# Optimization experiments

Measured on AMD Instinct MI355X. Metric: run time of the kernel, lower is better.

The kernel has to match this reference:

```python
import jax, jax.numpy as jnp
import numpy as np
import math

SEQ, BSZ, D, H, W = 2048, 2, 1024, 16, 8
HD = D // H          # head_dim = 64
P = SEQ // W         # phrase_num = 256 (seq divisible by window -> no pad needed)


def setup_inputs() -> dict:
    key = jax.random.key(0)
    ks = jax.random.split(key, 8)
    s = 1.0 / math.sqrt(D)
    def w(k):
        return jax.random.normal(k, (D, D), jnp.float32) * s
    zb = jnp.zeros((D,), jnp.float32)
    return {
        'query': jax.random.normal(ks[0], (SEQ, BSZ, D), jnp.float32),
        'Wq_base': w(ks[1]), 'bq_base': zb,
        'Wk_base': w(ks[2]), 'bk_base': zb,
        'Wq_gauss': w(ks[3]), 'bq_gauss': zb,
        'Wk_gauss': w(ks[4]), 'bk_gauss': zb,
        'Wv': w(ks[5]), 'bv': zb,
        'Wo': w(ks[6]), 'bo': zb,
    }


def reference(query, Wq_base, bq_base, Wk_base, bk_base,
              Wq_gauss, bq_gauss, Wk_gauss, bk_gauss, Wv, bv, Wo, bo):
    seq, bsz, d = query.shape
    scaling = HD ** -0.5

    def to_heads(x):  # (len, bsz, D) -> (bsz, H, len, HD)
        return x.reshape(x.shape[0], bsz, H, HD).transpose(1, 2, 0, 3)

    # ---- base multi-head attention branch ----
    q_b = to_heads(query @ Wq_base.T + bq_base) * scaling
    k_b = to_heads(query @ Wk_base.T + bk_base)
    v = to_heads(query @ Wv.T + bv)
    base_scores = jnp.einsum('bhid,bhjd->bhij', q_b, k_b)   # (B,H,S,S)
    attn_base = jax.nn.softmax(base_scores, axis=-1)

    # ---- phrase encoding: fixed windows + max pooling ----
    phrase = query.reshape(P, W, bsz, d).max(axis=1)        # (P, bsz, D)

    # ---- gaussian branch: query attends over phrase reps ----
    q_g = to_heads(query @ Wq_gauss.T + bq_gauss) * scaling
    k_g = (phrase @ Wk_gauss.T + bk_gauss).reshape(P, bsz, H, HD).transpose(1, 2, 0, 3)
    wts = jax.nn.softmax(jnp.einsum('bhid,bhpd->bhip', q_g, k_g), axis=-1)  # (B,H,S,P)

    # fixed Gaussians per phrase: mu at window center, sigma = window/4
    pos = jnp.arange(seq, dtype=jnp.float32)                     # key positions
    mu = jnp.arange(P, dtype=jnp.float32) * W + (W - 1) / 2.0    # (P,)
    sigma = W / 4.0
    gauss = jnp.exp(-(pos[None, :] - mu[:, None]) ** 2 / (2.0 * sigma * sigma)) \
            / (math.sqrt(2.0 * math.pi) * sigma)                 # (P, S)
    attn_gauss = jnp.einsum('bhip,pj->bhij', wts, gauss)         # (B,H,S,S)

    # combine the two attention distributions
    attn = 0.5 * (attn_base + attn_gauss)

    out = jnp.einsum('bhij,bhjd->bhid', attn, v)                 # (B,H,S,HD)
    out = out.transpose(2, 0, 1, 3).reshape(seq, bsz, d)         # (S,B,D)
    return out @ Wo.T + bo
```

## Files before the change

kernel.cpp:

```cpp
#include <hip/hip_runtime.h>
#include <hip/hip_bf16.h>

#define SEQ 2048
#define BSZ 2
#define DIM 1024
#define NH 16
#define HD 64
#define WIN 8
#define PN 256

typedef __hip_bfloat16 bf16;
typedef __attribute__((ext_vector_type(8))) short short8;
typedef __attribute__((ext_vector_type(4))) float f32x4;

__device__ __forceinline__ float b2f(bf16 x) { return __bfloat162float(x); }
__device__ __forceinline__ bf16 f2b(float x) { return __float2bfloat16(x); }
__device__ __forceinline__ short fbits(float x) { bf16 h = __float2bfloat16(x); return *(short*)&h; }

__device__ __forceinline__ void gl_lds16(const bf16* g, bf16* l) {
    __builtin_amdgcn_global_load_lds((const __attribute__((address_space(1))) void*)g,
                                     (__attribute__((address_space(3))) void*)l, 16, 0, 0);
}

__global__ void convert_kernel(const float* __restrict__ q,
                               const float* __restrict__ w0, const float* __restrict__ w1,
                               const float* __restrict__ w2, const float* __restrict__ w3,
                               const float* __restrict__ w4, const float* __restrict__ w5,
                               bf16* __restrict__ qbf, bf16* __restrict__ wbf) {
    int i = blockIdx.x * 256 + threadIdx.x;
    const int QV = (SEQ * BSZ * DIM) / 8;
    const int WV = (DIM * DIM) / 8;
    const float* src;
    bf16* dst;
    size_t off;
    if (i < QV) { src = q; dst = qbf; off = (size_t)i * 8; }
    else {
        int j = i - QV;
        int mat = j / WV, k = j - mat * WV;
        src = (mat == 0) ? w0 : (mat == 1) ? w1 : (mat == 2) ? w2
            : (mat == 3) ? w3 : (mat == 4) ? w4 : w5;
        dst = wbf + (size_t)mat * DIM * DIM;
        off = (size_t)k * 8;
    }
    f32x4 a = *(const f32x4*)(src + off);
    f32x4 b4 = *(const f32x4*)(src + off + 4);
    short8 o;
#pragma unroll
    for (int e = 0; e < 4; ++e) { o[e] = fbits(a[e]); o[e + 4] = fbits(b4[e]); }
    *(short8*)(dst + off) = o;
}

__global__ void bias_pack_kernel(const float* __restrict__ b0, const float* __restrict__ b1,
                                 const float* __restrict__ b2, const float* __restrict__ b3,
                                 const float* __restrict__ b4, const float* __restrict__ b5,
                                 float* __restrict__ bp) {
    int i = blockIdx.x * 256 + threadIdx.x;
    int mat = i >> 10, k = i & 1023;
    const float* s = (mat == 0) ? b0 : (mat == 1) ? b1 : (mat == 2) ? b2
                   : (mat == 3) ? b3 : (mat == 4) ? b4 : b5;
    bp[i] = s[k];
}

__global__ void phrase_max_kernel(const float* __restrict__ q, bf16* __restrict__ phrase) {
    int idx = blockIdx.x * 256 + threadIdx.x;
    int d  = idx % DIM;
    int pb = idx / DIM;
    int b  = pb % BSZ;
    int p  = pb / BSZ;
    float m = -1e30f;
#pragma unroll
    for (int w = 0; w < WIN; ++w)
        m = fmaxf(m, q[((size_t)(p * WIN + w) * BSZ + b) * DIM + d]);
    phrase[idx] = f2b(m);
}

__global__ void gauss_v_kernel(const bf16* __restrict__ vT, bf16* __restrict__ gvT) {
    int row = blockIdx.x;
    int p   = threadIdx.x;
    float mu = p * (float)WIN + (WIN - 1) * 0.5f;
    float acc = 0.f;
    int j0 = p * WIN - 12;
    const bf16* src = vT + (size_t)row * SEQ;
#pragma unroll
    for (int jj = 0; jj < 32; ++jj) {
        int j = j0 + jj;
        if (j < 0 || j >= SEQ) continue;
        float dd = (float)j - mu;
        acc += __expf(-dd * dd * 0.125f) * 0.199471140200716f * b2f(src[j]);
    }
    gvT[(size_t)row * PN + p] = f2b(acc);
}

__device__ __forceinline__ void gemm_body(const bf16* __restrict__ A,
                                          const bf16* __restrict__ W,
                                          const float* __restrict__ bias,
                                          void* __restrict__ Cout,
                                          int m0, int n0, float scale,
                                          int mode, int LEN) {
    __shared__ bf16 As[128 * 32];
    __shared__ bf16 Ws[128 * 32];
    int t = threadIdx.x;
    int wave = t >> 6, lane = t & 63;
    int wm = (wave >> 1) * 64, wn = (wave & 1) * 64;
    int l15 = lane & 15, quad = lane >> 4;

    f32x4 acc[4][4] = {};

    for (int k0 = 0; k0 < DIM; k0 += 32) {
        {
            int c0 = t, c1 = t + 256;
            gl_lds16(A + (size_t)(m0 + (c0 >> 2)) * DIM + k0 + (c0 & 3) * 8, &As[c0 * 8]);
            gl_lds16(A + (size_t)(m0 + (c1 >> 2)) * DIM + k0 + (c1 & 3) * 8, &As[c1 * 8]);
            gl_lds16(W + (size_t)(n0 + (c0 >> 2)) * DIM + k0 + (c0 & 3) * 8, &Ws[c0 * 8]);
            gl_lds16(W + (size_t)(n0 + (c1 >> 2)) * DIM + k0 + (c1 & 3) * 8, &Ws[c1 * 8]);
        }
        __syncthreads();
        short8 af[4], bfr[4];
#pragma unroll
        for (int tm = 0; tm < 4; ++tm)
            af[tm] = *(short8*)&As[(wm + tm * 16 + l15) * 32 + quad * 8];
#pragma unroll
        for (int tn = 0; tn < 4; ++tn)
            bfr[tn] = *(short8*)&Ws[(wn + tn * 16 + l15) * 32 + quad * 8];
#pragma unroll
        for (int tm = 0; tm < 4; ++tm)
#pragma unroll
            for (int tn = 0; tn < 4; ++tn)
                acc[tm][tn] = __builtin_amdgcn_mfma_f32_16x16x32_bf16(af[tm], bfr[tn], acc[tm][tn], 0, 0, 0);
        __syncthreads();
    }

#pragma unroll
    for (int tm = 0; tm < 4; ++tm) {
        int mrow = m0 + wm + tm * 16 + quad * 4;
#pragma unroll
        for (int tn = 0; tn < 4; ++tn) {
            int n = n0 + wn + tn * 16 + l15;
            float bsv = bias[n];
#pragma unroll
            for (int r = 0; r < 4; ++r) {
                int m = mrow + r;
                float val = (acc[tm][tn][r] + bsv) * scale;
                if (mode == 0) {
                    int s = m / BSZ, b = m % BSZ;
                    int h = n >> 6, hd = n & 63;
                    ((bf16*)Cout)[((size_t)(b * NH + h) * LEN + s) * HD + hd] = f2b(val);
                } else if (mode == 2) {
                    int s = m / BSZ, b = m % BSZ;
                    int h = n >> 6, hd = n & 63;
                    ((bf16*)Cout)[((size_t)(b * NH + h) * HD + hd) * LEN + s] = f2b(val);
                } else {
                    ((float*)Cout)[(size_t)m * DIM + n] = val;
                }
            }
        }
    }
}

#define QSCALE (0.125f * 1.44269504088896f)

__global__ __launch_bounds__(256) void gemm_proj(const bf16* __restrict__ qbf,
                                                 const bf16* __restrict__ phrasebf,
                                                 const bf16* __restrict__ wbf,
                                                 const float* __restrict__ bias_pack,
                                                 bf16* __restrict__ q_b, bf16* __restrict__ k_b,
                                                 bf16* __restrict__ vT, bf16* __restrict__ q_g,
                                                 bf16* __restrict__ k_g) {
    int z = blockIdx.z;
    const bf16* A = qbf;
    bf16* C;
    int mode = 0, LEN = SEQ;
    float scale = 1.0f;
    switch (z) {
        case 0: C = q_b; scale = QSCALE; break;
        case 1: C = k_b; break;
        case 2: C = vT; mode = 2; break;
        case 3: C = q_g; scale = QSCALE; break;
        default:
            if (blockIdx.x >= 4) return;
            A = phrasebf; C = k_g; LEN = PN; break;
    }
    gemm_body(A, wbf + (size_t)z * DIM * DIM, bias_pack + z * DIM, C,
              blockIdx.x * 128, blockIdx.y * 128, scale, mode, LEN);
}

__global__ __launch_bounds__(256) void gemm_final(const bf16* __restrict__ attn_bf,
                                                  const bf16* __restrict__ wbf,
                                                  const float* __restrict__ bias_pack,
                                                  float* __restrict__ out) {
    gemm_body(attn_bf, wbf + (size_t)5 * DIM * DIM, bias_pack + 5 * DIM, out,
              blockIdx.x * 128, blockIdx.y * 128, 1.0f, 1, SEQ);
}

__global__ __launch_bounds__(256) void attn_kernel(const bf16* __restrict__ qb,
                                                   const bf16* __restrict__ kb,
                                                   const bf16* __restrict__ vT,
                                                   const bf16* __restrict__ qg,
                                                   const bf16* __restrict__ kg,
                                                   const bf16* __restrict__ gvT,
                                                   bf16* __restrict__ out) {
    __shared__ bf16 Qs[64][72];
    __shared__ bf16 Ks[64][72];
    __shared__ bf16 Vt[64][72];
    __shared__ bf16 Ps[64][72];

    int t = threadIdx.x;
    int wave = t >> 6, lane = t & 63;
    int l15 = lane & 15, quad = lane >> 4;
    int q0 = blockIdx.x * 64;
    int bh = blockIdx.y;
    int b = bh / NH, h = bh % NH;

    const short8 ones = (short8)0x3F80;

    float result[4][4] = {};

    for (int phase = 0; phase < 2; ++phase) {
        const bf16* qptr = phase ? qb : qg;
        const bf16* kptr = phase ? kb : kg;
        const bf16* vtp  = phase ? vT : gvT;
        int kvlen = phase ? SEQ : PN;

        __syncthreads();
        {
            int r = t >> 2, c0 = (t & 3) * 16;
            const bf16* qsrc = qptr + ((size_t)bh * SEQ + q0 + r) * HD + c0;
            *(short8*)&Qs[r][c0]     = *(const short8*)qsrc;
            *(short8*)&Qs[r][c0 + 8] = *(const short8*)(qsrc + 8);
        }

        f32x4 o_acc[4] = {};
        f32x4 l_acc = {};
        int nchunk = kvlen / 64;
        for (int ch = 0; ch < nchunk; ++ch) {
            int j0 = ch * 64;
            __syncthreads();
            {
                int r = t >> 2, c0 = (t & 3) * 16;
                const bf16* ksrc = kptr + ((size_t)bh * kvlen + j0 + r) * HD + c0;
                const bf16* vsrc = vtp + (size_t)(bh * HD + r) * kvlen + j0 + c0;
                *(short8*)&Ks[r][c0]     = *(const short8*)ksrc;
                *(short8*)&Ks[r][c0 + 8] = *(const short8*)(ksrc + 8);
                *(short8*)&Vt[r][c0]     = *(const short8*)vsrc;
                *(short8*)&Vt[r][c0 + 8] = *(const short8*)(vsrc + 8);
            }
            __syncthreads();

            f32x4 s_acc[4] = {};
#pragma unroll
            for (int kk = 0; kk < 2; ++kk) {
                short8 a = *(short8*)&Qs[wave * 16 + l15][kk * 32 + quad * 8];
#pragma unroll
                for (int tn = 0; tn < 4; ++tn) {
                    short8 bb = *(short8*)&Ks[tn * 16 + l15][kk * 32 + quad * 8];
                    s_acc[tn] = __builtin_amdgcn_mfma_f32_16x16x32_bf16(a, bb, s_acc[tn], 0, 0, 0);
                }
            }
#pragma unroll
            for (int tn = 0; tn < 4; ++tn)
#pragma unroll
                for (int r = 0; r < 4; ++r)
                    Ps[wave * 16 + quad * 4 + r][tn * 16 + l15] =
                        f2b(exp2f(fminf(s_acc[tn][r], 43.f)));
#pragma unroll
            for (int kk = 0; kk < 2; ++kk) {
                short8 pa = *(short8*)&Ps[wave * 16 + l15][kk * 32 + quad * 8];
                l_acc = __builtin_amdgcn_mfma_f32_16x16x32_bf16(pa, ones, l_acc, 0, 0, 0);
#pragma unroll
                for (int tn = 0; tn < 4; ++tn) {
                    short8 vb = *(short8*)&Vt[tn * 16 + l15][kk * 32 + quad * 8];
                    o_acc[tn] = __builtin_amdgcn_mfma_f32_16x16x32_bf16(pa, vb, o_acc[tn], 0, 0, 0);
                }
            }
        }
#pragma unroll
        for (int r = 0; r < 4; ++r) {
            float inv = 0.5f / fmaxf(l_acc[r], 1e-30f);
#pragma unroll
            for (int tn = 0; tn < 4; ++tn)
                result[tn][r] += o_acc[tn][r] * inv;
        }
    }

#pragma unroll
    for (int r = 0; r < 4; ++r) {
        int srow = q0 + wave * 16 + quad * 4 + r;
        int m = srow * BSZ + b;
#pragma unroll
        for (int tn = 0; tn < 4; ++tn) {
            int dcol = h * HD + tn * 16 + l15;
            out[(size_t)m * DIM + dcol] = f2b(result[tn][r]);
        }
    }
}

extern "C" void kernel_launch(void* const* d_in, const int* in_sizes, int n_in,
                              void* d_out, int out_size, void* d_ws, size_t ws_size,
                              hipStream_t stream) {
    (void)in_sizes; (void)n_in; (void)out_size; (void)ws_size;
    const float* query = (const float*)d_in[0];
    const float* Wq_b  = (const float*)d_in[1];
    const float* bq_b  = (const float*)d_in[2];
    const float* Wk_b  = (const float*)d_in[3];
    const float* bk_b  = (const float*)d_in[4];
    const float* Wq_g  = (const float*)d_in[5];
    const float* bq_g  = (const float*)d_in[6];
    const float* Wk_g  = (const float*)d_in[7];
    const float* bk_g  = (const float*)d_in[8];
    const float* Wv    = (const float*)d_in[9];
    const float* bv    = (const float*)d_in[10];
    const float* Wo    = (const float*)d_in[11];
    const float* bo    = (const float*)d_in[12];
    float* out = (float*)d_out;

    const size_t NQ = (size_t)BSZ * NH * SEQ * HD;
    const size_t NP = (size_t)BSZ * NH * PN * HD;
    bf16* qbf      = (bf16*)d_ws;
    bf16* wbf      = qbf + NQ;
    bf16* phrasebf = wbf + (size_t)6 * DIM * DIM;
    bf16* q_b      = phrasebf + (size_t)PN * BSZ * DIM;
    bf16* k_b      = q_b + NQ;
    bf16* vT       = k_b + NQ;
    bf16* q_g      = vT + NQ;
    bf16* k_g      = q_g + NQ;
    bf16* gvT      = k_g + NP;
    bf16* attn_bf  = gvT + NP;
    float* bias_pack = (float*)(attn_bf + NQ);

    const int QV = (SEQ * BSZ * DIM) / 8, WV6 = 6 * (DIM * DIM) / 8;
    convert_kernel<<<(QV + WV6) / 256, 256, 0, stream>>>(
        query, Wq_b, Wk_b, Wv, Wq_g, Wk_g, Wo, qbf, wbf);
    bias_pack_kernel<<<24, 256, 0, stream>>>(bq_b, bk_b, bv, bq_g, bk_g, bo, bias_pack);
    phrase_max_kernel<<<(PN * BSZ * DIM) / 256, 256, 0, stream>>>(query, phrasebf);

    dim3 gp((SEQ * BSZ) / 128, DIM / 128, 5);
    gemm_proj<<<gp, 256, 0, stream>>>(qbf, phrasebf, wbf, bias_pack,
                                      q_b, k_b, vT, q_g, k_g);

    gauss_v_kernel<<<BSZ * NH * HD, PN, 0, stream>>>(vT, gvT);

    dim3 g3(SEQ / 64, BSZ * NH);
    attn_kernel<<<g3, 256, 0, stream>>>(q_b, k_b, vT, q_g, k_g, gvT, attn_bf);

    dim3 gf((SEQ * BSZ) / 128, DIM / 128);
    gemm_final<<<gf, 256, 0, stream>>>(attn_bf, wbf, bias_pack, out);
}
```

Before: 298.3 us.

## Double query tile in attention, register-prefetch K/V, fold bias pack into convert

The attention kernel now handles 128 query rows per block, two 16-row MFMA tiles per wave, so each K/V chunk loaded into LDS is reused twice as much. Global loads for the next K/V chunk are issued into registers before the current chunk's compute so their latency overlaps with the MFMAs. The separate bias-pack kernel is merged into the convert kernel as extra blocks, removing one launch. In exchange the attention grid is halved to 512 blocks, which lowers occupancy, and register pressure and LDS use both rise.

```diff
diff --git a/kernel.cpp b/kernel.cpp
--- a/kernel.cpp
+++ b/kernel.cpp
@@ -26,10 +26,25 @@
                                const float* __restrict__ w0, const float* __restrict__ w1,
                                const float* __restrict__ w2, const float* __restrict__ w3,
                                const float* __restrict__ w4, const float* __restrict__ w5,
-                               bf16* __restrict__ qbf, bf16* __restrict__ wbf) {
+                               const float* __restrict__ b0, const float* __restrict__ b1,
+                               const float* __restrict__ b2, const float* __restrict__ b3,
+                               const float* __restrict__ b4, const float* __restrict__ b5,
+                               bf16* __restrict__ qbf, bf16* __restrict__ wbf,
+                               float* __restrict__ bp) {
     int i = blockIdx.x * 256 + threadIdx.x;
     const int QV = (SEQ * BSZ * DIM) / 8;
     const int WV = (DIM * DIM) / 8;
+    const int TV = QV + 6 * WV;
+    if (i >= TV) {
+        int j = i - TV;
+        if (j >= 768) return;
+        int mat = j >> 7, k = (j & 127) * 8;
+        const float* s = (mat == 0) ? b0 : (mat == 1) ? b1 : (mat == 2) ? b2
+                       : (mat == 3) ? b3 : (mat == 4) ? b4 : b5;
+        *(f32x4*)(bp + mat * DIM + k)     = *(const f32x4*)(s + k);
+        *(f32x4*)(bp + mat * DIM + k + 4) = *(const f32x4*)(s + k + 4);
+        return;
+    }
     const float* src;
     bf16* dst;
     size_t off;
@@ -42,23 +57,12 @@
         dst = wbf + (size_t)mat * DIM * DIM;
         off = (size_t)k * 8;
     }
-    f32x4 a = *(const f32x4*)(src + off);
-    f32x4 b4 = *(const f32x4*)(src + off + 4);
+    f32x4 av4 = *(const f32x4*)(src + off);
+    f32x4 bv4 = *(const f32x4*)(src + off + 4);
     short8 o;
 #pragma unroll
-    for (int e = 0; e < 4; ++e) { o[e] = fbits(a[e]); o[e + 4] = fbits(b4[e]); }
+    for (int e = 0; e < 4; ++e) { o[e] = fbits(av4[e]); o[e + 4] = fbits(bv4[e]); }
     *(short8*)(dst + off) = o;
-}
-
-__global__ void bias_pack_kernel(const float* __restrict__ b0, const float* __restrict__ b1,
-                                 const float* __restrict__ b2, const float* __restrict__ b3,
-                                 const float* __restrict__ b4, const float* __restrict__ b5,
-                                 float* __restrict__ bp) {
-    int i = blockIdx.x * 256 + threadIdx.x;
-    int mat = i >> 10, k = i & 1023;
-    const float* s = (mat == 0) ? b0 : (mat == 1) ? b1 : (mat == 2) ? b2
-                   : (mat == 3) ? b3 : (mat == 4) ? b4 : b5;
-    bp[i] = s[k];
 }
 
 __global__ void phrase_max_kernel(const float* __restrict__ q, bf16* __restrict__ phrase) {
@@ -199,99 +203,123 @@
                                                    const bf16* __restrict__ kg,
                                                    const bf16* __restrict__ gvT,
                                                    bf16* __restrict__ out) {
-    __shared__ bf16 Qs[64][72];
+    __shared__ bf16 Qs[128][72];
     __shared__ bf16 Ks[64][72];
     __shared__ bf16 Vt[64][72];
-    __shared__ bf16 Ps[64][72];
+    __shared__ bf16 Ps[128][72];
 
     int t = threadIdx.x;
     int wave = t >> 6, lane = t & 63;
     int l15 = lane & 15, quad = lane >> 4;
-    int q0 = blockIdx.x * 64;
+    int q0 = blockIdx.x * 128;
     int bh = blockIdx.y;
     int b = bh / NH, h = bh % NH;
 
     const short8 ones = (short8)0x3F80;
 
-    float result[4][4] = {};
+    float result[2][4][4] = {};
 
     for (int phase = 0; phase < 2; ++phase) {
         const bf16* qptr = phase ? qb : qg;
         const bf16* kptr = phase ? kb : kg;
         const bf16* vtp  = phase ? vT : gvT;
         int kvlen = phase ? SEQ : PN;
+        int nchunk = kvlen / 64;
 
         __syncthreads();
         {
-            int r = t >> 2, c0 = (t & 3) * 16;
+            int r = t >> 1, c0 = (t & 1) * 32;
             const bf16* qsrc = qptr + ((size_t)bh * SEQ + q0 + r) * HD + c0;
-            *(short8*)&Qs[r][c0]     = *(const short8*)qsrc;
-            *(short8*)&Qs[r][c0 + 8] = *(const short8*)(qsrc + 8);
-        }
-
-        f32x4 o_acc[4] = {};
-        f32x4 l_acc = {};
-        int nchunk = kvlen / 64;
+#pragma unroll
+            for (int e = 0; e < 4; ++e)
+                *(short8*)&Qs[r][c0 + e * 8] = *(const short8*)(qsrc + e * 8);
+        }
+
+        int sr = t >> 2, sc = (t & 3) * 16;
+        const bf16* kbase = kptr + ((size_t)bh * kvlen + sr) * HD + sc;
+        const bf16* vbase = vtp + (size_t)(bh * HD + sr) * kvlen + sc;
+
+        short8 kr0, kr1, vr0, vr1;
+        kr0 = *(const short8*)(kbase);
+        kr1 = *(const short8*)(kbase + 8);
+        vr0 = *(const short8*)(vbase);
+        vr1 = *(const short8*)(vbase + 8);
+
+        f32x4 o_acc[2][4] = {};
+        f32x4 l_acc[2] = {};
         for (int ch = 0; ch < nchunk; ++ch) {
-            int j0 = ch * 64;
             __syncthreads();
-            {
-                int r = t >> 2, c0 = (t & 3) * 16;
-                const bf16* ksrc = kptr + ((size_t)bh * kvlen + j0 + r) * HD + c0;
-                const bf16* vsrc = vtp + (size_t)(bh * HD + r) * kvlen + j0 + c0;
-                *(short8*)&Ks[r][c0]     = *(const short8*)ksrc;
-                *(short8*)&Ks[r][c0 + 8] = *(const short8*)(ksrc + 8);
-                *(short8*)&Vt[r][c0]     = *(const short8*)vsrc;
-                *(short8*)&Vt[r][c0 + 8] = *(const short8*)(vsrc + 8);
+            *(short8*)&Ks[sr][sc]     = kr0;
+            *(short8*)&Ks[sr][sc + 8] = kr1;
+            *(short8*)&Vt[sr][sc]     = vr0;
+            *(short8*)&Vt[sr][sc + 8] = vr1;
+            if (ch + 1 < nchunk) {
+                const bf16* kn = kbase + (size_t)(ch + 1) * 64 * HD;
+                const bf16* vn = vbase + (ch + 1) * 64;
+                kr0 = *(const short8*)(kn);
+                kr1 = *(const short8*)(kn + 8);
+                vr0 = *(const short8*)(vn);
+                vr1 = *(const short8*)(vn + 8);
             }
             __syncthreads();
 
-            f32x4 s_acc[4] = {};
+            f32x4 s_acc[2][4] = {};
 #pragma unroll
             for (int kk = 0; kk < 2; ++kk) {
-                short8 a = *(short8*)&Qs[wave * 16 + l15][kk * 32 + quad * 8];
+                short8 a0 = *(short8*)&Qs[wave * 32 + l15][kk * 32 + quad * 8];
+                short8 a1 = *(short8*)&Qs[wave * 32 + 16 + l15][kk * 32 + quad * 8];
 #pragma unroll
                 for (int tn = 0; tn < 4; ++tn) {
                     short8 bb = *(short8*)&Ks[tn * 16 + l15][kk * 32 + quad * 8];
-                    s_acc[tn] = __builtin_amdgcn_mfma_f32_16x16x32_bf16(a, bb, s_acc[tn], 0, 0, 0);
+                    s_acc[0][tn] = __builtin_amdgcn_mfma_f32_16x16x32_bf16(a0, bb, s_acc[0][tn], 0, 0, 0);
+                    s_acc[1][tn] = __builtin_amdgcn_mfma_f32_16x16x32_bf16(a1, bb, s_acc[1][tn], 0, 0, 0);
                 }
             }
 #pragma unroll
-            for (int tn = 0; tn < 4; ++tn)
-#pragma unroll
-                for (int r = 0; r < 4; ++r)
-                    Ps[wave * 16 + quad * 4 + r][tn * 16 + l15] =
-                        f2b(exp2f(fminf(s_acc[tn][r], 43.f)));
+            for (int m = 0; m < 2; ++m)
+#pragma unroll
+                for (int tn = 0; tn < 4; ++tn)
+#pragma unroll
+                    for (int r = 0; r < 4; ++r)
+                        Ps[wave * 32 + m * 16 + quad * 4 + r][tn * 16 + l15] =
+                            f2b(exp2f(fminf(s_acc[m][tn][r], 43.f)));
 #pragma unroll
             for (int kk = 0; kk < 2; ++kk) {
-                short8 pa = *(short8*)&Ps[wave * 16 + l15][kk * 32 + quad * 8];
-                l_acc = __builtin_amdgcn_mfma_f32_16x16x32_bf16(pa, ones, l_acc, 0, 0, 0);
+                short8 pa0 = *(short8*)&Ps[wave * 32 + l15][kk * 32 + quad * 8];
+                short8 pa1 = *(short8*)&Ps[wave * 32 + 16 + l15][kk * 32 + quad * 8];
+                l_acc[0] = __builtin_amdgcn_mfma_f32_16x16x32_bf16(pa0, ones, l_acc[0], 0, 0, 0);
+                l_acc[1] = __builtin_amdgcn_mfma_f32_16x16x32_bf16(pa1, ones, l_acc[1], 0, 0, 0);
 #pragma unroll
                 for (int tn = 0; tn < 4; ++tn) {
                     short8 vb = *(short8*)&Vt[tn * 16 + l15][kk * 32 + quad * 8];
-                    o_acc[tn] = __builtin_amdgcn_mfma_f32_16x16x32_bf16(pa, vb, o_acc[tn], 0, 0, 0);
+                    o_acc[0][tn] = __builtin_amdgcn_mfma_f32_16x16x32_bf16(pa0, vb, o_acc[0][tn], 0, 0, 0);
+                    o_acc[1][tn] = __builtin_amdgcn_mfma_f32_16x16x32_bf16(pa1, vb, o_acc[1][tn], 0, 0, 0);
                 }
             }
         }
 #pragma unroll
+        for (int m = 0; m < 2; ++m)
+#pragma unroll
+            for (int r = 0; r < 4; ++r) {
+                float inv = 0.5f / fmaxf(l_acc[m][r], 1e-30f);
+#pragma unroll
+                for (int tn = 0; tn < 4; ++tn)
+                    result[m][tn][r] += o_acc[m][tn][r] * inv;
+            }
+    }
+
+#pragma unroll
+    for (int m = 0; m < 2; ++m)
+#pragma unroll
         for (int r = 0; r < 4; ++r) {
-            float inv = 0.5f / fmaxf(l_acc[r], 1e-30f);
-#pragma unroll
-            for (int tn = 0; tn < 4; ++tn)
-                result[tn][r] += o_acc[tn][r] * inv;
-        }
-    }
-
-#pragma unroll
-    for (int r = 0; r < 4; ++r) {
-        int srow = q0 + wave * 16 + quad * 4 + r;
-        int m = srow * BSZ + b;
-#pragma unroll
-        for (int tn = 0; tn < 4; ++tn) {
-            int dcol = h * HD + tn * 16 + l15;
-            out[(size_t)m * DIM + dcol] = f2b(result[tn][r]);
-        }
-    }
+            int srow = q0 + wave * 32 + m * 16 + quad * 4 + r;
+            int mm = srow * BSZ + b;
+#pragma unroll
+            for (int tn = 0; tn < 4; ++tn) {
+                int dcol = h * HD + tn * 16 + l15;
+                out[(size_t)mm * DIM + dcol] = f2b(result[m][tn][r]);
+            }
+        }
 }
 
 extern "C" void kernel_launch(void* const* d_in, const int* in_sizes, int n_in,
@@ -328,9 +356,9 @@
     float* bias_pack = (float*)(attn_bf + NQ);
 
     const int QV = (SEQ * BSZ * DIM) / 8, WV6 = 6 * (DIM * DIM) / 8;
-    convert_kernel<<<(QV + WV6) / 256, 256, 0, stream>>>(
-        query, Wq_b, Wk_b, Wv, Wq_g, Wk_g, Wo, qbf, wbf);
-    bias_pack_kernel<<<24, 256, 0, stream>>>(bq_b, bk_b, bv, bq_g, bk_g, bo, bias_pack);
+    convert_kernel<<<(QV + WV6) / 256 + 3, 256, 0, stream>>>(
+        query, Wq_b, Wk_b, Wv, Wq_g, Wk_g, Wo,
+        bq_b, bk_b, bv, bq_g, bk_g, bo, qbf, wbf, bias_pack);
     phrase_max_kernel<<<(PN * BSZ * DIM) / 256, 256, 0, stream>>>(query, phrasebf);
 
     dim3 gp((SEQ * BSZ) / 128, DIM / 128, 5);
@@ -339,7 +367,7 @@
 
     gauss_v_kernel<<<BSZ * NH * HD, PN, 0, stream>>>(vT, gvT);
 
-    dim3 g3(SEQ / 64, BSZ * NH);
+    dim3 g3(SEQ / 128, BSZ * NH);
     attn_kernel<<<g3, 256, 0, stream>>>(q_b, k_b, vT, q_g, k_g, gvT, attn_bf);
 
     dim3 gf((SEQ * BSZ) / 128, DIM / 128);
```

New measurement: 325.0 us. +9.0%, slower.
